# Kernel tuning notes

Hardware: AMD Instinct MI355X
Metric: run time of the kernel (lower is better)

The kernel has to match this reference:

```python
import jax, jax.numpy as jnp
import numpy as np

H, B, G, NQ = 8, 16, 512, 512
D, KD, VD, E = 512, 64, 64, 512
NORM = 1.0 / np.sqrt(KD)


def _unif(key, shape):
    stdv = 1.0 / np.sqrt(shape[-1])
    return jax.random.uniform(key, shape, jnp.float32, -stdv, stdv)


def setup_inputs() -> dict:
    key = jax.random.key(0)
    ks = jax.random.split(key, 20)
    inp = {
        "q": jax.random.normal(ks[0], (B, NQ, D), jnp.float32),
        "att_masks": jax.random.bernoulli(ks[1], 0.5, (B, G, NQ)),
        "group_masks": jax.random.bernoulli(ks[2], 0.5, (B, NQ, G)),
        "sparse_dist_masks": jax.random.bernoulli(ks[3], 0.5, (B, NQ, G)),
    }
    wnames = ["W_query", "W_K", "W_V", "W_Q_ps", "W_K_ps", "W_V_ps",
              "W_Q_sp", "W_K_sp", "W_V_sp", "W_Q_pg", "W_K_pg", "W_V_pg"]
    for i, n in enumerate(wnames):
        kd = KD if ("V" not in n or "query" in n) else VD  # key_dim == val_dim here
        inp[n] = _unif(ks[4 + i], (H, D, kd))
    inp["W_out"] = _unif(ks[16], (H, KD, E))
    return inp


def _forward(q, att_masks, group_masks, sparse_dist_masks,
             W_query, W_K, W_V, W_Q_ps, W_K_ps, W_V_ps,
             W_Q_sp, W_K_sp, W_V_sp, W_Q_pg, W_K_pg, W_V_pg, W_out):
    h = q  # h=None -> h=q in original

    def proj(x, W):  # (B,N,D) x (H,D,K) -> (H,B,N,K)
        return jnp.einsum('bnd,hdk->hbnk', x, W)

    def branch(Wq, Wk, Wv):
        Q = proj(q, Wq)
        K = proj(h, Wk)
        V = proj(h, Wv)
        s = NORM * jnp.einsum('hbqk,hbgk->hbqg', Q, K)  # (H,B,Nq,G)
        return s, V

    s0, V0 = branch(W_query, W_K, W_V)
    s1, V1 = branch(W_Q_ps, W_K_ps, W_V_ps)
    s2, V2 = branch(W_Q_sp, W_K_sp, W_V_sp)
    s3, V3 = branch(W_Q_pg, W_K_pg, W_V_pg)

    m0 = sparse_dist_masks                      # (B,Nq,G)
    m1 = jnp.swapaxes(att_masks, 1, 2)          # transpose(1,2) -> (B,Nq,G)
    m2 = att_masks.reshape(B, NQ, G)            # raw view (Nq==G)
    m3 = group_masks

    scores = jnp.concatenate([s0, s1, s2, s3], axis=-1)        # (H,B,Nq,4G)
    masks = jnp.concatenate([m0, m1, m2, m3], axis=-1)[None]   # (1,B,Nq,4G)

    # torch.sparse.softmax over nonzero (= unmasked) entries; masked stay 0
    neg = jnp.where(masks, scores, -jnp.inf)
    mx = jnp.max(neg, axis=-1, keepdims=True)
    mx = jnp.where(jnp.isfinite(mx), mx, 0.0)
    ex = jnp.where(masks, jnp.exp(neg - mx), 0.0)
    den = jnp.sum(ex, axis=-1, keepdims=True)
    attn = jnp.where(den > 0, ex / jnp.where(den > 0, den, 1.0), 0.0)

    attn = attn.reshape(H, B, NQ, 4, G)                 # (H,B,Nq,4,G)
    Vs = jnp.stack([V0, V1, V2, V3], axis=0)            # (4,H,B,G,Vd)
    heads = jnp.einsum('hbqcg,chbgv->hbqv', attn, Vs)   # (H,B,Nq,Vd)

    out = jnp.einsum('hbqv,hve->bqe', heads, W_out)     # (B,Nq,E)
    return out


def reference(q, att_masks, group_masks, sparse_dist_masks,
              W_query, W_K, W_V, W_Q_ps, W_K_ps, W_V_ps,
              W_Q_sp, W_K_sp, W_V_sp, W_Q_pg, W_K_pg, W_V_pg, W_out):
    return _forward(q, att_masks, group_masks, sparse_dist_masks,
                    W_query, W_K, W_V, W_Q_ps, W_K_ps, W_V_ps,
                    W_Q_sp, W_K_sp, W_V_sp, W_Q_pg, W_K_pg, W_V_pg, W_out)
```

## Files before the change

### kernel.cpp

```cpp
#include <hip/hip_runtime.h>

using u8 = unsigned char;
using u16 = unsigned short;
using u32 = unsigned int;
using u64 = unsigned long long;

typedef __attribute__((ext_vector_type(8))) __bf16 bf16x8;
typedef __attribute__((ext_vector_type(2))) __bf16 bf16x2;
typedef __attribute__((ext_vector_type(8))) u16 u16x8;
typedef __attribute__((ext_vector_type(4))) float f32x4;
typedef __attribute__((ext_vector_type(2))) float f32x2;
typedef __attribute__((ext_vector_type(2))) u32 u32x2;

#define MFMA16(A, B, C) __builtin_amdgcn_mfma_f32_16x16x32_bf16((A), (B), (C), 0, 0, 0)

#if __has_builtin(__builtin_amdgcn_exp2f)
#define EXP2(x) __builtin_amdgcn_exp2f(x)
#else
#define EXP2(x) __expf((x)*0.69314718055994531f)
#endif

__device__ __forceinline__ u16 f2bf(float f) {
  u32 u = __builtin_bit_cast(u32, f);
  u += 0x7fffu + ((u >> 16) & 1u);
  return (u16)(u >> 16);
}

__device__ __forceinline__ void gl_lds16(const void* g, void* l) {
  __builtin_amdgcn_global_load_lds(
      (const __attribute__((address_space(1))) void*)g,
      (__attribute__((address_space(3))) void*)l, 16, 0, 0);
}


struct PrepArgs {
  const float* q; const int* att; const int* grp; const int* sd;
  const float* w[12]; const float* wout;
  u16* qb; u16* Wbt; u16* Wot; u64* RB;
};

__global__ __launch_bounds__(256) void prep_all_k(PrepArgs a) {
  int bid = blockIdx.x;
  int t = threadIdx.x;
  if (bid < 64) {
    int h = bid >> 3, e0 = (bid & 7) * 64;
    int ep = t >> 2;
    int vc = t & 3;
    const float* src = a.wout + ((size_t)(h * 64)) * 512 + e0 + ep;
#pragma unroll
    for (int j = 0; j < 2; j++) {
      int v0 = vc * 16 + j * 8;
      u32 w0 = f2bf(src[(size_t)(v0 + 0) * 512]) | ((u32)f2bf(src[(size_t)(v0 + 1) * 512]) << 16);
      u32 w1 = f2bf(src[(size_t)(v0 + 2) * 512]) | ((u32)f2bf(src[(size_t)(v0 + 3) * 512]) << 16);
      u32 w2 = f2bf(src[(size_t)(v0 + 4) * 512]) | ((u32)f2bf(src[(size_t)(v0 + 5) * 512]) << 16);
      u32 w3 = f2bf(src[(size_t)(v0 + 6) * 512]) | ((u32)f2bf(src[(size_t)(v0 + 7) * 512]) << 16);
      *(uint4*)&a.Wot[((size_t)(h * 512 + e0 + ep)) * 64 + v0] = make_uint4(w0, w1, w2, w3);
    }
  } else if (bid < 576) {
    int nb = bid - 64;
    int b = nb >> 5, rest = nb & 31;
    int gc = rest >> 2, qq = rest & 3;
    int wave = t >> 6, lane = t & 63;
    const int* col = a.att + ((size_t)(b * 512 + gc * 64 + lane)) * 512;
    int qbase = qq * 128 + wave * 32;
#pragma unroll 8
    for (int qi = 0; qi < 32; qi++) {
      int q = qbase + qi;
      u64 m = __ballot(col[q] != 0);
      if (lane == 0) a.RB[((size_t)(b * 4 + 1) * 512 + q) * 8 + gc] = m;
    }
  } else if (bid < 672) {
    int nb = bid - 576;
    int iw = nb >> 3;
    int h  = nb & 7;
    int kk = t & 63;
    int dd = t >> 6;
    float scale = ((iw % 3) == 0) ? 0.18033688011112042f : 1.0f;
    const float* W = a.w[iw];
    for (int d = dd; d < 512; d += 4) {
      float v = W[((size_t)(h * 512 + d)) * 64 + kk] * scale;
      a.Wbt[((size_t)(iw * 512 + h * 64 + kk)) * 512 + d] = f2bf(v);
    }
  } else if (bid < 1184) {
    int nb = bid - 672;
    int wave = t >> 6, lane = t & 63;
    int b = nb >> 5, qc = nb & 31;
    int q0 = qc * 16 + wave * 4;
#pragma unroll
    for (int r = 0; r < 4; r++) {
      int q = q0 + r;
      size_t rbase = ((size_t)(b * 512 + q)) * 512;
#pragma unroll
      for (int gc = 0; gc < 8; gc++) {
        u64 m0 = __ballot(a.sd [rbase + gc * 64 + lane] != 0);
        u64 m2 = __ballot(a.att[rbase + gc * 64 + lane] != 0);
        u64 m3 = __ballot(a.grp[rbase + gc * 64 + lane] != 0);
        if (lane == 0) {
          size_t ob = ((size_t)(b * 4) * 512 + q) * 8 + gc;
          a.RB[ob]            = m0;
          a.RB[ob + 2 * 4096] = m2;
          a.RB[ob + 3 * 4096] = m3;
        }
      }
    }
  } else {
    int idx = (bid - 1184) * 256 + t;
    const float4* p = (const float4*)a.q + (size_t)idx * 2;
    float4 x = p[0], y = p[1];
    u32 w0 = f2bf(x.x) | ((u32)f2bf(x.y) << 16);
    u32 w1 = f2bf(x.z) | ((u32)f2bf(x.w) << 16);
    u32 w2 = f2bf(y.x) | ((u32)f2bf(y.y) << 16);
    u32 w3 = f2bf(y.z) | ((u32)f2bf(y.w) << 16);
    ((uint4*)a.qb)[idx] = make_uint4(w0, w1, w2, w3);
  }
}

__global__ __launch_bounds__(256) void gemm_proj_k(const u16* __restrict__ qb,
                                                   const u16* __restrict__ Wbt,
                                                   u16* __restrict__ P) {
  __shared__ __align__(16) u16 smem[17408];
  u16* As = smem;
  u16* Bs = smem + 8192;
  int t = threadIdx.x;
  int wave = t >> 6, lane = t & 63, quad = lane >> 4, l16 = lane & 15;
  int m0w = (wave >> 1) * 64, n0w = (wave & 1) * 64;
  int bm = blockIdx.x, bn = blockIdx.y;
  f32x4 acc[4][4] = {};
  int lr8 = lane >> 3;
  int lc8 = (lane & 7) ^ lr8;
  const u16* ag = qb  + ((size_t)(bm * 128 + wave * 32 + lr8)) * 512 + lc8 * 8;
  const u16* bg = Wbt + ((size_t)(bn * 128 + wave * 32 + lr8)) * 512 + lc8 * 8;
  char* AsB = (char*)As;
  char* BsB = (char*)Bs;
  int stO = wave * 4096 + lane * 16;

  uint4 sA0, sA1, sA2, sA3, sB0, sB1, sB2, sB3;
#define GLD(k0_) {                                          \
    sA0 = *(const uint4*)(ag + 0 * 4096 + (k0_));           \
    sA1 = *(const uint4*)(ag + 1 * 4096 + (k0_));           \
    sA2 = *(const uint4*)(ag + 2 * 4096 + (k0_));           \
    sA3 = *(const uint4*)(ag + 3 * 4096 + (k0_));           \
    sB0 = *(const uint4*)(bg + 0 * 4096 + (k0_));           \
    sB1 = *(const uint4*)(bg + 1 * 4096 + (k0_));           \
    sB2 = *(const uint4*)(bg + 2 * 4096 + (k0_));           \
    sB3 = *(const uint4*)(bg + 3 * 4096 + (k0_)); }
#define GST() {                                             \
    *(uint4*)(AsB + stO)        = sA0;                      \
    *(uint4*)(AsB + stO + 1024) = sA1;                      \
    *(uint4*)(AsB + stO + 2048) = sA2;                      \
    *(uint4*)(AsB + stO + 3072) = sA3;                      \
    *(uint4*)(BsB + stO)        = sB0;                      \
    *(uint4*)(BsB + stO + 1024) = sB1;                      \
    *(uint4*)(BsB + stO + 2048) = sB2;                      \
    *(uint4*)(BsB + stO + 3072) = sB3; }

  GLD(0);
  GST();
  __syncthreads();

  for (int ks = 0; ks < 8; ks++) {
    int k0 = ks * 64;
    if (ks < 7) GLD(k0 + 64);
#pragma unroll
    for (int kc = 0; kc < 2; kc++) {
      bf16x8 am[4], bnf[4];
#pragma unroll
      for (int i = 0; i < 4; i++) {
        int ca = ((kc * 4 + quad) ^ (l16 & 7)) * 8;
        am[i]  = *(const bf16x8*)&As[(m0w + i * 16 + l16) * 64 + ca];
        bnf[i] = *(const bf16x8*)&Bs[(n0w + i * 16 + l16) * 64 + ca];
      }
#pragma unroll
      for (int mt = 0; mt < 4; mt++)
#pragma unroll
        for (int nt = 0; nt < 4; nt++)
          acc[mt][nt] = MFMA16(am[mt], bnf[nt], acc[mt][nt]);
    }
    if (ks < 7) {
      __syncthreads();
      GST();
      __syncthreads();
    }
  }
  int iw = bn >> 2;
  bool isV = (iw % 3) == 2;
  int b  = bm >> 2;
  int n0 = (bm & 3) * 128;
  u16 (*Cs)[136] = (u16(*)[136])smem;
  __syncthreads();
#pragma unroll
  for (int mt = 0; mt < 4; mt++)
#pragma unroll
    for (int nt = 0; nt < 4; nt++)
#pragma unroll
      for (int r = 0; r < 4; r++) {
        int rm = m0w + mt * 16 + quad * 4 + r;
        int cn = n0w + nt * 16 + l16;
        u16 v = f2bf(acc[mt][nt][r]);
        if (!isV) Cs[rm][cn] = v;
        else      Cs[cn][rm] = v;
      }
  __syncthreads();
#pragma unroll
  for (int p = 0; p < 8; p++) {
    int idx = p * 256 + t;
    int seg  = idx & 15;
    int crow = idx >> 4;
    uint4 v = *(const uint4*)&Cs[crow][seg * 8];
    if (!isV) {
      int col = seg * 8;
      int cg = col >> 6, k = col & 63;
      int h = (bn * 2 + cg) & 7;
      u16* dst = P + ((size_t)((iw * 8 + h) * 16 + b)) * 32768 + (size_t)(n0 + crow) * 64 + k;
      *(uint4*)dst = v;
    } else {
      int cg = crow >> 6, k = crow & 63;
      int h = (bn * 2 + cg) & 7;
      u16* dst = P + ((size_t)((iw * 8 + h) * 16 + b)) * 32768 + (size_t)k * 512 + n0 + seg * 8;
      *(uint4*)dst = v;
    }
  }
}

__global__ __launch_bounds__(256) void attn_k(const u16* __restrict__ P,
                                              const u64* __restrict__ RB,
                                              u16* __restrict__ heads) {
  __shared__ __align__(16) u16 QPs[4096];
  __shared__ __align__(16) u16 Ks[4096];
  __shared__ __align__(16) u16 Vs[4096];
  __shared__ __align__(16) u64 Ms[64][10];
  int t = threadIdx.x;
  int wave = t >> 6, lane = t & 63, quad = lane >> 4, l16 = lane & 15;
  int id = blockIdx.x;
  int r8 = id & 7, kk2 = id >> 3;
  int bh = ((kk2 >> 3) << 3) | r8;
  int qt = kk2 & 7;
  int b = bh & 15, h = bh >> 4;
  int q0 = qt * 64;
  int lr8 = lane >> 3, lc8 = (lane & 7) ^ lr8;
  f32x4 O0 = {}, O1 = {}, O2 = {}, O3 = {};
  f32x4 Oden = {};
  u16x8 ov = {0x3F80, 0x3F80, 0x3F80, 0x3F80, 0x3F80, 0x3F80, 0x3F80, 0x3F80};
  bf16x8 ones = __builtin_bit_cast(bf16x8, ov);

  uint4 rK0, rK1, rV0, rV1, rQ0, rQ1, rM;
  char* KsB = (char*)Ks;
  char* VsB = (char*)Vs;
  char* QsB = (char*)QPs;
  int stOff = (wave * 16 + lr8) * 128 + (lane & 7) * 16;

#define LOADKV(c, g0) {                                                              \
    const u16* PK_ = P + ((size_t)((3 * (c) + 1) * 8 + h) * 16 + b) * 32768;         \
    const u16* PV_ = P + ((size_t)((3 * (c) + 2) * 8 + h) * 16 + b) * 32768;         \
    rK0 = *(const uint4*)(PK_ + (size_t)((g0) + wave * 16 + lr8) * 64 + lc8 * 8);    \
    rK1 = *(const uint4*)(PK_ + (size_t)((g0) + wave * 16 + 8 + lr8) * 64 + lc8 * 8);\
    rV0 = *(const uint4*)(PV_ + (size_t)(wave * 16 + lr8) * 512 + (g0) + lc8 * 8);   \
    rV1 = *(const uint4*)(PV_ + (size_t)(wave * 16 + 8 + lr8) * 512 + (g0) + lc8 * 8);}
#define STOREKV() {                                                                  \
    *(uint4*)(KsB + stOff)        = rK0;                                             \
    *(uint4*)(KsB + stOff + 1024) = rK1;                                             \
    *(uint4*)(VsB + stOff)        = rV0;                                             \
    *(uint4*)(VsB + stOff + 1024) = rV1; }
#define LOADQM(c) {                                                                  \
    const u16* PQ_ = P + ((size_t)((3 * (c)) * 8 + h) * 16 + b) * 32768;             \
    rQ0 = *(const uint4*)(PQ_ + (size_t)(q0 + wave * 16 + lr8) * 64 + lc8 * 8);      \
    rQ1 = *(const uint4*)(PQ_ + (size_t)(q0 + wave * 16 + 8 + lr8) * 64 + lc8 * 8);  \
    rM  = *(const uint4*)(RB + ((size_t)((b * 4 + (c)) * 512 + q0 + (t >> 2))) * 8 + (t & 3) * 2); }
#define STOREQM() {                                                                  \
    *(uint4*)(QsB + stOff)        = rQ0;                                             \
    *(uint4*)(QsB + stOff + 1024) = rQ1;                                             \
    *(uint4*)((char*)Ms + (t >> 2) * 80 + (t & 3) * 16) = rM; }

  LOADKV(0, 0);
  LOADQM(0);
  STOREKV();
  STOREQM();
  __syncthreads();

  bf16x8 aq0, aq1;
  for (int tt = 0; tt < 32; tt++) {
    int gt = tt & 7;
    if (gt == 0) {
      aq0 = *(const bf16x8*)&QPs[(wave * 16 + l16) * 64 + ((quad) ^ (l16 & 7)) * 8];
      aq1 = *(const bf16x8*)&QPs[(wave * 16 + l16) * 64 + ((4 + quad) ^ (l16 & 7)) * 8];
    }
    int nxt = tt + 1;
    int nc = nxt >> 3, ngt = nxt & 7;
    if (nxt < 32) {
      LOADKV(nc, ngt * 64);
      if (ngt == 0) LOADQM(nc);
    }
    f32x4 S0, S1, S2, S3;
#define QKNT(Sn, nt) {                                                                \
      bf16x8 bk0_ = *(const bf16x8*)&Ks[((nt) * 16 + l16) * 64 + ((quad) ^ (l16 & 7)) * 8];     \
      bf16x8 bk1_ = *(const bf16x8*)&Ks[((nt) * 16 + l16) * 64 + ((4 + quad) ^ (l16 & 7)) * 8]; \
      f32x4 sa_ = {};                                                                 \
      sa_ = MFMA16(bk0_, aq0, sa_);                                                   \
      sa_ = MFMA16(bk1_, aq1, sa_);                                                   \
      Sn = sa_; }
    QKNT(S0, 0) QKNT(S1, 1) QKNT(S2, 2) QKNT(S3, 3)
    {
      u64 m = Ms[wave * 16 + l16][gt];
      u32 mlo = (u32)m, mhi = (u32)(m >> 32);
      int shq = quad * 4;
      u32 tb0 = mlo >> shq, tb1 = mlo >> (shq + 16);
      u32 tb2 = mhi >> shq, tb3 = mhi >> (shq + 16);
      char* PsB = (char*)QPs + (wave * 16 + l16) * 128 + (quad & 1) * 8;
#define PPACK(Sn, tn, nt) {                                                           \
        f32x2 p0_ = {EXP2(Sn[0]), EXP2(Sn[1])};                                       \
        f32x2 p1_ = {EXP2(Sn[2]), EXP2(Sn[3])};                                       \
        u32 w0_ = __builtin_bit_cast(u32, __builtin_convertvector(p0_, bf16x2));      \
        u32 w1_ = __builtin_bit_cast(u32, __builtin_convertvector(p1_, bf16x2));      \
        u32 ma_ = (u32)((int)((tn) << 31) >> 31);                                     \
        u32 mb_ = (u32)((int)((tn) << 30) >> 31);                                     \
        u32 mc_ = (u32)((int)((tn) << 29) >> 31);                                     \
        u32 md_ = (u32)((int)((tn) << 28) >> 31);                                     \
        w0_ &= (ma_ & 0x0000ffffu) | (mb_ & 0xffff0000u);                             \
        w1_ &= (mc_ & 0x0000ffffu) | (md_ & 0xffff0000u);                             \
        u32x2 wp_ = {w0_, w1_};                                                       \
        int ch_ = ((nt) * 2 + (quad >> 1)) ^ (l16 & 7);                               \
        *(u32x2*)(PsB + ch_ * 16) = wp_; }
      PPACK(S0, tb0, 0) PPACK(S1, tb1, 1) PPACK(S2, tb2, 2) PPACK(S3, tb3, 3)
    }
#define PVKC(kc) {                                                                    \
      bf16x8 ap_ = *(const bf16x8*)&QPs[(wave * 16 + l16) * 64 + ((((kc) * 4 + quad) ^ (l16 & 7)) * 8)]; \
      bf16x8 bv0_ = *(const bf16x8*)&Vs[(0 * 16 + l16) * 64 + ((((kc) * 4 + quad) ^ (l16 & 7)) * 8)];    \
      bf16x8 bv1_ = *(const bf16x8*)&Vs[(1 * 16 + l16) * 64 + ((((kc) * 4 + quad) ^ (l16 & 7)) * 8)];    \
      bf16x8 bv2_ = *(const bf16x8*)&Vs[(2 * 16 + l16) * 64 + ((((kc) * 4 + quad) ^ (l16 & 7)) * 8)];    \
      bf16x8 bv3_ = *(const bf16x8*)&Vs[(3 * 16 + l16) * 64 + ((((kc) * 4 + quad) ^ (l16 & 7)) * 8)];    \
      O0 = MFMA16(ap_, bv0_, O0);                                                     \
      O1 = MFMA16(ap_, bv1_, O1);                                                     \
      O2 = MFMA16(ap_, bv2_, O2);                                                     \
      O3 = MFMA16(ap_, bv3_, O3);                                                     \
      Oden = MFMA16(ap_, ones, Oden); }
    PVKC(0) PVKC(1)
    __syncthreads();
    if (nxt < 32) {
      STOREKV();
      if (ngt == 0) STOREQM();
    }
    __syncthreads();
  }
#pragma unroll
  for (int r = 0; r < 4; r++) {
    float den = Oden[r];
    float i0 = (den > 0.f) ? O0[r] / den : 0.f;
    float i1 = (den > 0.f) ? O1[r] / den : 0.f;
    float i2 = (den > 0.f) ? O2[r] / den : 0.f;
    float i3 = (den > 0.f) ? O3[r] / den : 0.f;
    size_t base = ((size_t)(h * 16 + b) * 512 + q0 + wave * 16 + quad * 4 + r) * 64 + l16;
    heads[base + 0]  = f2bf(i0);
    heads[base + 16] = f2bf(i1);
    heads[base + 32] = f2bf(i2);
    heads[base + 48] = f2bf(i3);
  }
}

__global__ __launch_bounds__(256) void gemm_out_k(const u16* __restrict__ heads,
                                                  const u16* __restrict__ Wot,
                                                  float* __restrict__ out) {
  __shared__ __align__(16) u16 As[4096];
  __shared__ __align__(16) u16 Bs[4096];
  int t = threadIdx.x;
  int wave = t >> 6, lane = t & 63, quad = lane >> 4, l16 = lane & 15;
  int m0 = blockIdx.x * 64, e0 = blockIdx.y * 64;
  int b = m0 >> 9, q0 = m0 & 511;
  int lr8 = lane >> 3, lc8 = (lane & 7) ^ lr8;
  f32x4 acc[4] = {};
  char* AsB = (char*)As;
  char* BsB = (char*)Bs;
  int stO = wave * 2048 + lane * 16;
  const u16* hg = heads + ((size_t)(b * 512) + q0 + wave * 16 + lr8) * 64 + lc8 * 8;
  const u16* wg = Wot + ((size_t)(e0 + wave * 16 + lr8)) * 64 + lc8 * 8;

  uint4 gA0, gA1, gB0, gB1;
#define GO_LD(h_) {                                                        \
    gA0 = *(const uint4*)(hg + (size_t)(h_) * 524288);                     \
    gA1 = *(const uint4*)(hg + (size_t)(h_) * 524288 + 512);               \
    gB0 = *(const uint4*)(wg + (size_t)(h_) * 32768);                      \
    gB1 = *(const uint4*)(wg + (size_t)(h_) * 32768 + 512); }
#define GO_ST() {                                                          \
    *(uint4*)(AsB + stO)        = gA0;                                     \
    *(uint4*)(AsB + stO + 1024) = gA1;                                     \
    *(uint4*)(BsB + stO)        = gB0;                                     \
    *(uint4*)(BsB + stO + 1024) = gB1; }

  GO_LD(0);
  GO_ST();
  __syncthreads();

  for (int h = 0; h < 8; h++) {
    if (h < 7) GO_LD(h + 1);
#pragma unroll
    for (int kc = 0; kc < 2; kc++) {
      bf16x8 af = *(const bf16x8*)&As[(wave * 16 + l16) * 64 + ((kc * 4 + quad) ^ (l16 & 7)) * 8];
#pragma unroll
      for (int nt = 0; nt < 4; nt++) {
        bf16x8 bfr = *(const bf16x8*)&Bs[(nt * 16 + l16) * 64 + ((kc * 4 + quad) ^ (l16 & 7)) * 8];
        acc[nt] = MFMA16(af, bfr, acc[nt]);
      }
    }
    if (h < 7) {
      __syncthreads();
      GO_ST();
      __syncthreads();
    }
  }
#pragma unroll
  for (int nt = 0; nt < 4; nt++)
#pragma unroll
    for (int r = 0; r < 4; r++)
      out[((size_t)(b * 512 + q0 + wave * 16 + quad * 4 + r)) * 512 + e0 + nt * 16 + l16] = acc[nt][r];
}


extern "C" void kernel_launch(void* const* d_in, const int* in_sizes, int n_in,
                              void* d_out, int out_size, void* d_ws, size_t ws_size,
                              hipStream_t stream) {
  char* ws = (char*)d_ws;
  u16* qb    = (u16*)(ws + 0);
  u16* Wbt   = (u16*)(ws + 8388608);
  u16* Wot   = (u16*)(ws + 14680064);
  u64* RB    = (u64*)(ws + 15204352);
  u16* P     = (u16*)(ws + 17301504);
  u16* heads = (u16*)(ws + 117964800);
  float* out = (float*)d_out;

  PrepArgs pa;
  pa.q   = (const float*)d_in[0];
  pa.att = (const int*)d_in[1];
  pa.grp = (const int*)d_in[2];
  pa.sd  = (const int*)d_in[3];
  for (int j = 0; j < 12; j++) pa.w[j] = (const float*)d_in[4 + j];
  pa.wout = (const float*)d_in[16];
  pa.qb = qb; pa.Wbt = Wbt; pa.Wot = Wot; pa.RB = RB;

  prep_all_k<<<3232, 256, 0, stream>>>(pa);
  gemm_proj_k<<<dim3(64, 48), 256, 0, stream>>>(qb, Wbt, P);
  attn_k<<<1024, 256, 0, stream>>>(P, RB, heads);
  gemm_out_k<<<dim3(128, 8), 256, 0, stream>>>(heads, Wot, out);
}
```

Baseline: 350.8 us.

## Derive transposed att mask bitmap from packed bits and vectorize weight conversion

Stops reading the full int32 att_masks tensor a second time with a strided column access to build the transposed mask bitmap. A new small kernel builds it by bit-transposing the already packed row bitmap with wave ballots. The weight transpose and bf16 conversion now write 16-byte packed stores over more blocks instead of scattered 2-byte stores, and the prep blocks are reordered. This costs an extra kernel launch plus a dependency between the prep and pack kernels.

```diff
diff --git a/kernel.cpp b/kernel.cpp
--- a/kernel.cpp
+++ b/kernel.cpp
@@ -39,52 +39,12 @@
   u16* qb; u16* Wbt; u16* Wot; u64* RB;
 };
 
-__global__ __launch_bounds__(256) void prep_all_k(PrepArgs a) {
+__global__ __launch_bounds__(256) void prep_main_k(PrepArgs a) {
   int bid = blockIdx.x;
   int t = threadIdx.x;
-  if (bid < 64) {
-    int h = bid >> 3, e0 = (bid & 7) * 64;
-    int ep = t >> 2;
-    int vc = t & 3;
-    const float* src = a.wout + ((size_t)(h * 64)) * 512 + e0 + ep;
-#pragma unroll
-    for (int j = 0; j < 2; j++) {
-      int v0 = vc * 16 + j * 8;
-      u32 w0 = f2bf(src[(size_t)(v0 + 0) * 512]) | ((u32)f2bf(src[(size_t)(v0 + 1) * 512]) << 16);
-      u32 w1 = f2bf(src[(size_t)(v0 + 2) * 512]) | ((u32)f2bf(src[(size_t)(v0 + 3) * 512]) << 16);
-      u32 w2 = f2bf(src[(size_t)(v0 + 4) * 512]) | ((u32)f2bf(src[(size_t)(v0 + 5) * 512]) << 16);
-      u32 w3 = f2bf(src[(size_t)(v0 + 6) * 512]) | ((u32)f2bf(src[(size_t)(v0 + 7) * 512]) << 16);
-      *(uint4*)&a.Wot[((size_t)(h * 512 + e0 + ep)) * 64 + v0] = make_uint4(w0, w1, w2, w3);
-    }
-  } else if (bid < 576) {
-    int nb = bid - 64;
-    int b = nb >> 5, rest = nb & 31;
-    int gc = rest >> 2, qq = rest & 3;
+  if (bid < 512) {
     int wave = t >> 6, lane = t & 63;
-    const int* col = a.att + ((size_t)(b * 512 + gc * 64 + lane)) * 512;
-    int qbase = qq * 128 + wave * 32;
-#pragma unroll 8
-    for (int qi = 0; qi < 32; qi++) {
-      int q = qbase + qi;
-      u64 m = __ballot(col[q] != 0);
-      if (lane == 0) a.RB[((size_t)(b * 4 + 1) * 512 + q) * 8 + gc] = m;
-    }
-  } else if (bid < 672) {
-    int nb = bid - 576;
-    int iw = nb >> 3;
-    int h  = nb & 7;
-    int kk = t & 63;
-    int dd = t >> 6;
-    float scale = ((iw % 3) == 0) ? 0.18033688011112042f : 1.0f;
-    const float* W = a.w[iw];
-    for (int d = dd; d < 512; d += 4) {
-      float v = W[((size_t)(h * 512 + d)) * 64 + kk] * scale;
-      a.Wbt[((size_t)(iw * 512 + h * 64 + kk)) * 512 + d] = f2bf(v);
-    }
-  } else if (bid < 1184) {
-    int nb = bid - 672;
-    int wave = t >> 6, lane = t & 63;
-    int b = nb >> 5, qc = nb & 31;
+    int b = bid >> 5, qc = bid & 31;
     int q0 = qc * 16 + wave * 4;
 #pragma unroll
     for (int r = 0; r < 4; r++) {
@@ -103,8 +63,51 @@
         }
       }
     }
+  } else if (bid < 896) {
+    int nb = bid - 512;
+    int iw = nb >> 5;
+    int rest = nb & 31;
+    int h = rest >> 2;
+    int d0 = (rest & 3) * 128;
+    int kk = t & 63;
+    int db0 = t >> 6;
+    float scale = ((iw % 3) == 0) ? 0.18033688011112042f : 1.0f;
+    const float* W = a.w[iw] + ((size_t)(h * 512)) * 64 + kk;
+    u16* dst = a.Wbt + ((size_t)(iw * 512 + h * 64 + kk)) * 512;
+#pragma unroll
+    for (int it = 0; it < 4; it++) {
+      int d = d0 + (db0 + it * 4) * 8;
+      float v0 = W[(size_t)(d + 0) * 64] * scale;
+      float v1 = W[(size_t)(d + 1) * 64] * scale;
+      float v2 = W[(size_t)(d + 2) * 64] * scale;
+      float v3 = W[(size_t)(d + 3) * 64] * scale;
+      float v4 = W[(size_t)(d + 4) * 64] * scale;
+      float v5 = W[(size_t)(d + 5) * 64] * scale;
+      float v6 = W[(size_t)(d + 6) * 64] * scale;
+      float v7 = W[(size_t)(d + 7) * 64] * scale;
+      u32 w0 = f2bf(v0) | ((u32)f2bf(v1) << 16);
+      u32 w1 = f2bf(v2) | ((u32)f2bf(v3) << 16);
+      u32 w2 = f2bf(v4) | ((u32)f2bf(v5) << 16);
+      u32 w3 = f2bf(v6) | ((u32)f2bf(v7) << 16);
+      *(uint4*)(dst + d) = make_uint4(w0, w1, w2, w3);
+    }
+  } else if (bid < 960) {
+    int nb = bid - 896;
+    int h = nb >> 3, e0 = (nb & 7) * 64;
+    int ep = t >> 2;
+    int vc = t & 3;
+    const float* src = a.wout + ((size_t)(h * 64)) * 512 + e0 + ep;
+#pragma unroll
+    for (int j = 0; j < 2; j++) {
+      int v0 = vc * 16 + j * 8;
+      u32 w0 = f2bf(src[(size_t)(v0 + 0) * 512]) | ((u32)f2bf(src[(size_t)(v0 + 1) * 512]) << 16);
+      u32 w1 = f2bf(src[(size_t)(v0 + 2) * 512]) | ((u32)f2bf(src[(size_t)(v0 + 3) * 512]) << 16);
+      u32 w2 = f2bf(src[(size_t)(v0 + 4) * 512]) | ((u32)f2bf(src[(size_t)(v0 + 5) * 512]) << 16);
+      u32 w3 = f2bf(src[(size_t)(v0 + 6) * 512]) | ((u32)f2bf(src[(size_t)(v0 + 7) * 512]) << 16);
+      *(uint4*)&a.Wot[((size_t)(h * 512 + e0 + ep)) * 64 + v0] = make_uint4(w0, w1, w2, w3);
+    }
   } else {
-    int idx = (bid - 1184) * 256 + t;
+    int idx = (bid - 960) * 256 + t;
     const float4* p = (const float4*)a.q + (size_t)idx * 2;
     float4 x = p[0], y = p[1];
     u32 w0 = f2bf(x.x) | ((u32)f2bf(x.y) << 16);
@@ -113,6 +116,21 @@
     u32 w3 = f2bf(y.z) | ((u32)f2bf(y.w) << 16);
     ((uint4*)a.qb)[idx] = make_uint4(w0, w1, w2, w3);
   }
+}
+
+__global__ __launch_bounds__(256) void pack_cols_t_k(u64* __restrict__ RB) {
+  int t = threadIdx.x;
+  int wave = t >> 6, lane = t & 63;
+  int tile = blockIdx.x * 4 + wave;
+  int b = tile >> 6, qc = (tile >> 3) & 7, gc = tile & 7;
+  u64 R = RB[((size_t)(b * 4 + 2) * 512 + gc * 64 + lane) * 8 + qc];
+  u64 out = 0;
+#pragma unroll
+  for (int j = 0; j < 64; j++) {
+    u64 bal = __ballot(((R >> j) & 1) != 0);
+    if (lane == j) out = bal;
+  }
+  RB[((size_t)(b * 4 + 1) * 512 + qc * 64 + lane) * 8 + gc] = out;
 }
 
 __global__ __launch_bounds__(256) void gemm_proj_k(const u16* __restrict__ qb,
@@ -435,7 +453,8 @@
   pa.wout = (const float*)d_in[16];
   pa.qb = qb; pa.Wbt = Wbt; pa.Wot = Wot; pa.RB = RB;
 
-  prep_all_k<<<3232, 256, 0, stream>>>(pa);
+  prep_main_k<<<3008, 256, 0, stream>>>(pa);
+  pack_cols_t_k<<<256, 256, 0, stream>>>(RB);
   gemm_proj_k<<<dim3(64, 48), 256, 0, stream>>>(qb, Wbt, P);
   attn_k<<<1024, 256, 0, stream>>>(P, RB, heads);
   gemm_out_k<<<dim3(128, 8), 256, 0, stream>>>(heads, Wot, out);
```

After: 295.7 us (median of 2 runs). -15.7%, faster.
